# Kernel optimization log

Measured on AMD Instinct MI355X. Metric: run time of the kernel, lower is better.

Reference implementation:

```python
import jax, jax.numpy as jnp
import numpy as np

EMB, NH, NG, T_MAX = 2048, 16, 4, 2048
HD = EMB // NH          # 128
HPG = NH // NG          # 4
B, T = 2, 2048


def _rope_tables(t):
    inv_freq = 1.0 / (10000.0 ** (jnp.arange(0, HD, 2, dtype=jnp.float32) / HD))
    freqs = jnp.outer(jnp.arange(t, dtype=jnp.float32), inv_freq)  # [t, HD//2]
    return jnp.cos(freqs), jnp.sin(freqs)


def _apply_rope(x, cos, sin):
    # x: [..., t, HD], interleaved pairs (0::2 real, 1::2 imag)
    x1 = x[..., 0::2]
    x2 = x[..., 1::2]
    r1 = x1 * cos - x2 * sin
    r2 = x1 * sin + x2 * cos
    return jnp.stack([r1, r2], axis=-1).reshape(x.shape)


def setup_inputs() -> dict:
    key = jax.random.key(0)
    ks = jax.random.split(key, 5)
    s = 0.02
    return {
        "x": jax.random.normal(ks[0], (B, T, EMB), dtype=jnp.float32),
        "Wq": jax.random.normal(ks[1], (EMB, EMB), dtype=jnp.float32) * s,
        "Wk": jax.random.normal(ks[2], (NG * HD, EMB), dtype=jnp.float32) * s,
        "Wv": jax.random.normal(ks[3], (NG * HD, EMB), dtype=jnp.float32) * s,
        "Wo": jax.random.normal(ks[4], (EMB, EMB), dtype=jnp.float32) * s,
    }


def reference(x, Wq, Wk, Wv, Wo):
    b, t, _ = x.shape
    cos, sin = _rope_tables(t)  # [t, HD//2] each; broadcast over batch/heads

    # projections (torch Linear: x @ W.T)
    q = (x @ Wq.T).reshape(b, t, NH, HD).transpose(0, 2, 1, 3)  # [b, NH, t, HD]
    k = (x @ Wk.T).reshape(b, t, NG, HD).transpose(0, 2, 1, 3)  # [b, NG, t, HD]
    v = (x @ Wv.T).reshape(b, t, NG, HD).transpose(0, 2, 1, 3)  # [b, NG, t, HD]

    q = _apply_rope(q, cos, sin)
    k = _apply_rope(k, cos, sin)

    # grouped attention without materializing expanded K/V
    qg = q.reshape(b, NG, HPG, t, HD)                       # [b, g, h, t, d]
    scale = 1.0 / jnp.sqrt(jnp.asarray(HD, dtype=x.dtype))
    scores = jnp.einsum('bghtd,bgsd->bghts', qg, k) * scale  # [b, g, h, t, s]

    causal = jnp.tril(jnp.ones((t, t), dtype=bool))
    scores = jnp.where(causal, scores, jnp.finfo(scores.dtype).min)
    attn = jax.nn.softmax(scores, axis=-1)

    out = jnp.einsum('bghts,bgsd->bghtd', attn, v)           # [b, g, h, t, d]
    out = out.reshape(b, NH, t, HD).transpose(0, 2, 1, 3).reshape(b, t, EMB)
    return out @ Wo.T
```

## Files before the change

### kernel.cpp

```cpp
#include <hip/hip_runtime.h>
#include <stdint.h>
#include <math.h>

#define EMB 2048
#define NHq 16
#define NGk 4
#define HD 128
#define Bb 2
#define Tt 2048
#define MROWS (Bb*Tt)
#define QKVN 3072
#define NQT 32

typedef __bf16 bf16x8 __attribute__((ext_vector_type(8)));
typedef float f32x4 __attribute__((ext_vector_type(4)));
typedef unsigned int u32x4 __attribute__((ext_vector_type(4)));
typedef unsigned short u16;
typedef unsigned int u32;

__device__ __forceinline__ u16 f2bf(float f) {
    unsigned int u = __float_as_uint(f);
    u += 0x7fff + ((u >> 16) & 1);
    return (u16)(u >> 16);
}
__device__ __forceinline__ float bf2f(u16 u) {
    return __uint_as_float(((u32)u) << 16);
}
__device__ __forceinline__ u32 cvt_pk_bf16(float lo, float hi) {
    u32 r;
    asm("v_cvt_pk_bf16_f32 %0, %1, %2" : "=v"(r) : "v"(lo), "v"(hi));
    return r;
}

#define GLOAD_LDS16(g, l) \
    __builtin_amdgcn_global_load_lds((const __attribute__((address_space(1))) void*)(g), \
                                     (__attribute__((address_space(3))) void*)(l), 16, 0, 0)

__global__ void cast_bf16_kernel(const float* __restrict__ src, u16* __restrict__ dst, int n4) {
    int i = blockIdx.x * blockDim.x + threadIdx.x;
    if (i < n4) {
        float4 v = reinterpret_cast<const float4*>(src)[i];
        ushort4 o;
        o.x = f2bf(v.x); o.y = f2bf(v.y); o.z = f2bf(v.z); o.w = f2bf(v.w);
        reinterpret_cast<ushort4*>(dst)[i] = o;
    }
}

__global__ void wcast_kernel(const float* __restrict__ Wq, const float* __restrict__ Wk,
                             const float* __restrict__ Wv, const float* __restrict__ Wo,
                             u16* __restrict__ dst) {
    int i = blockIdx.x * blockDim.x + threadIdx.x;
    const float* src; int local;
    if (i < 1048576)      { src = Wq; local = i; }
    else if (i < 1310720) { src = Wk; local = i - 1048576; }
    else if (i < 1572864) { src = Wv; local = i - 1310720; }
    else                  { src = Wo; local = i - 1572864; }
    float4 v = reinterpret_cast<const float4*>(src)[local];
    ushort4 o;
    o.x = f2bf(v.x); o.y = f2bf(v.y); o.z = f2bf(v.z); o.w = f2bf(v.w);
    reinterpret_cast<ushort4*>(dst)[i] = o;
}

__global__ void rope_tables_kernel(float* __restrict__ ctab, float* __restrict__ stab) {
    int t = blockIdx.x, i = threadIdx.x;
    float inv = powf(10000.f, -2.f * (float)i / (float)HD);
    float ang = (float)t * inv;
    ctab[t * 64 + i] = cosf(ang);
    stab[t * 64 + i] = sinf(ang);
}

__global__ void rope_qk_kernel(const u16* __restrict__ lin, const float* __restrict__ ctab,
                               const float* __restrict__ stab, u16* __restrict__ Qb,
                               u16* __restrict__ Kb, float qscale) {
    int i = threadIdx.x;
    int tt = blockIdx.x * 4 + threadIdx.y;
    int hh = blockIdx.y, b = blockIdx.z;
    int coloff; u16* out; float scale;
    if (hh < NHq) { coloff = hh * HD; scale = qscale;
                    out = Qb + (((size_t)(b * NHq + hh)) * Tt + tt) * HD; }
    else { int g = hh - NHq; coloff = EMB + g * HD; scale = 1.f;
           out = Kb + (((size_t)(b * NGk + g)) * Tt + tt) * HD; }
    u32 pair = *reinterpret_cast<const u32*>(&lin[((size_t)(b * Tt + tt)) * QKVN + coloff + 2 * i]);
    float x1 = bf2f((u16)(pair & 0xffff)), x2 = bf2f((u16)(pair >> 16));
    float c = ctab[tt * 64 + i], s = stab[tt * 64 + i];
    ushort2 o;
    o.x = f2bf((x1 * c - x2 * s) * scale);
    o.y = f2bf((x1 * s + x2 * c) * scale);
    *reinterpret_cast<ushort2*>(&out[2 * i]) = o;
}

__global__ void vtrans_kernel(const u16* __restrict__ lin, u16* __restrict__ vt) {
    int tx = threadIdx.x, dy = threadIdx.y;
    int tt = blockIdx.x * 64 + tx;
    int g = blockIdx.y, b = blockIdx.z;
    int ttp = (tt & ~31) | (((tt >> 2) & 3) * 8 + ((tt >> 4) & 1) * 4 + (tt & 3));
    const u16* src = &lin[((size_t)(b * Tt + tt)) * QKVN + EMB + NGk * HD + g * HD];
    u16* dst = &vt[(((size_t)(b * NGk + g)) * HD) * Tt + ttp];
    #pragma unroll
    for (int k = 0; k < 16; ++k) {
        int d = dy + k * 8;
        dst[(size_t)d * Tt] = src[d];
    }
}

template<int OUTBF>
__global__ __launch_bounds__(256) void gemm_bt(const u16* __restrict__ A, const u16* __restrict__ W,
                                               void* __restrict__ Cout, int M, int N, int K) {
    __shared__ u16 Atile[128 * 32];
    __shared__ u16 Btile[128 * 32];
    const int brow = blockIdx.x * 128;
    const int bcol = blockIdx.y * 128;
    const int t = threadIdx.x;
    const int w = t >> 6, l = t & 63;
    const int lr = l & 15, lq = l >> 4;
    const int wr = (w >> 1) * 64, wc = (w & 1) * 64;
    f32x4 acc[4][4] = {};
    const int nkt = K >> 5;
    for (int kt = 0; kt < nkt; ++kt) {
        const int k0 = kt * 32;
        #pragma unroll
        for (int i = 0; i < 2; ++i) {
            int f = i * 256 + t;
            int row = f >> 2, cb = (f & 3) * 8;
            GLOAD_LDS16(A + (size_t)(brow + row) * K + k0 + cb, &Atile[(i * 256 + w * 64) * 8]);
            GLOAD_LDS16(W + (size_t)(bcol + row) * K + k0 + cb, &Btile[(i * 256 + w * 64) * 8]);
        }
        __syncthreads();
        bf16x8 a[4], b[4];
        #pragma unroll
        for (int m = 0; m < 4; ++m)
            a[m] = *reinterpret_cast<const bf16x8*>(&Atile[(wr + m * 16 + lr) * 32 + lq * 8]);
        #pragma unroll
        for (int n = 0; n < 4; ++n)
            b[n] = *reinterpret_cast<const bf16x8*>(&Btile[(wc + n * 16 + lr) * 32 + lq * 8]);
        #pragma unroll
        for (int m = 0; m < 4; ++m)
            #pragma unroll
            for (int n = 0; n < 4; ++n)
                acc[m][n] = __builtin_amdgcn_mfma_f32_16x16x32_bf16(a[m], b[n], acc[m][n], 0, 0, 0);
        __syncthreads();
    }
    #pragma unroll
    for (int m = 0; m < 4; ++m)
        #pragma unroll
        for (int n = 0; n < 4; ++n)
            #pragma unroll
            for (int r = 0; r < 4; ++r) {
                size_t idx = (size_t)(brow + wr + m * 16 + lq * 4 + r) * N + bcol + wc + n * 16 + lr;
                if (OUTBF) ((u16*)Cout)[idx] = f2bf(acc[m][n][r]);
                else       ((float*)Cout)[idx] = acc[m][n][r];
            }
}

__global__ __launch_bounds__(256) void flash_attn(const u16* __restrict__ Q, const u16* __restrict__ K,
                                                  const u16* __restrict__ Vt, u16* __restrict__ Out) {
    __shared__ __align__(16) char smem[65536];
    const int h = blockIdx.y;
    const int b = blockIdx.z;
    const int qt = (b == 0) ? blockIdx.x : (15 - blockIdx.x);
    const int g = h >> 2;
    const int t = threadIdx.x;
    const int w = t >> 6, l = t & 63;
    const int lr = l & 15, lq = l >> 4;
    const int qbase = qt * 128 + w * 32;

    const size_t qhead = ((size_t)(b * NHq + h)) * Tt;
    bf16x8 qf0[4], qf1[4];
    #pragma unroll
    for (int d = 0; d < 4; ++d) {
        qf0[d] = *reinterpret_cast<const bf16x8*>(&Q[(qhead + qbase + lr) * HD + d * 32 + lq * 8]);
        qf1[d] = *reinterpret_cast<const bf16x8*>(&Q[(qhead + qbase + 16 + lr) * HD + d * 32 + lq * 8]);
    }
    bf16x8 ones;
    #pragma unroll
    for (int j = 0; j < 8; ++j) ones[j] = (__bf16)1.0f;

    f32x4 o0[8] = {}, o1[8] = {};
    f32x4 ls0 = {}, ls1 = {};

    const int q0 = qbase + lr;
    const int q1 = qbase + 16 + lr;
    const int lastvis = (qbase + 31) >> 6;
    const size_t kbase  = ((size_t)(b * NGk + g)) * Tt * HD;
    const size_t vtbase = ((size_t)(b * NGk + g)) * HD * Tt;
    const int nkt = 2 * (qt + 1);

    int kofs[4], vofs[4];
    #pragma unroll
    for (int j = 0; j < 4; ++j) {
        int krow = j * 16 + (t >> 4);
        kofs[j] = krow * HD + (((t & 15) ^ (krow & 7)) * 8);
        int vrow = j * 32 + (t >> 3);
        vofs[j] = vrow * (int)Tt + (((t & 7) ^ (vrow & 7)) * 8);
    }

    #pragma unroll
    for (int j = 0; j < 4; ++j) {
        GLOAD_LDS16(K + kbase + kofs[j], smem + (j * 256 + t) * 16);
        GLOAD_LDS16(Vt + vtbase + vofs[j], smem + 32768 + (j * 256 + t) * 16);
    }

    for (int kt = 0; kt < nkt; ++kt) {
        __syncthreads();
        if (kt + 1 < nkt) {
            const size_t kp1 = (size_t)(kt + 1) * 64;
            char* kd = smem + ((kt + 1) & 1) * 16384;
            char* vd = smem + 32768 + ((kt + 1) & 1) * 16384;
            #pragma unroll
            for (int j = 0; j < 4; ++j) {
                GLOAD_LDS16(K + kbase + kp1 * HD + kofs[j], kd + (j * 256 + t) * 16);
                GLOAD_LDS16(Vt + vtbase + kp1 + vofs[j], vd + (j * 256 + t) * 16);
            }
        }
        if (kt > lastvis) continue;
        const char* Kb = smem + (kt & 1) * 16384;
        const char* Vb = smem + 32768 + (kt & 1) * 16384;

        f32x4 s0[4] = {}, s1[4] = {};
        __builtin_amdgcn_s_setprio(1);
        #pragma unroll
        for (int ct = 0; ct < 4; ++ct) {
            #pragma unroll
            for (int d = 0; d < 4; ++d) {
                int row = ct * 16 + lr;
                int bo = row * 256 + ((d * 64 + lq * 16) ^ ((row & 7) << 4));
                bf16x8 kf = *reinterpret_cast<const bf16x8*>(Kb + bo);
                s0[ct] = __builtin_amdgcn_mfma_f32_16x16x32_bf16(kf, qf0[d], s0[ct], 0, 0, 0);
                s1[ct] = __builtin_amdgcn_mfma_f32_16x16x32_bf16(kf, qf1[d], s1[ct], 0, 0, 0);
            }
        }
        __builtin_amdgcn_s_setprio(0);

        const bool diag = (kt == lastvis);
        const int kvb = kt * 64 + lq * 4;
        bf16x8 pf0[2], pf1[2];
        {
            float e[4][4];
            #pragma unroll
            for (int ct = 0; ct < 4; ++ct)
                #pragma unroll
                for (int r = 0; r < 4; ++r)
                    e[ct][r] = exp2f(s0[ct][r]);
            if (diag) {
                #pragma unroll
                for (int ct = 0; ct < 4; ++ct)
                    #pragma unroll
                    for (int r = 0; r < 4; ++r)
                        if (kvb + ct * 16 + r > q0) e[ct][r] = 0.f;
            }
            #pragma unroll
            for (int ks = 0; ks < 2; ++ks) {
                u32x4 pk;
                pk[0] = cvt_pk_bf16(e[ks * 2][0], e[ks * 2][1]);
                pk[1] = cvt_pk_bf16(e[ks * 2][2], e[ks * 2][3]);
                pk[2] = cvt_pk_bf16(e[ks * 2 + 1][0], e[ks * 2 + 1][1]);
                pk[3] = cvt_pk_bf16(e[ks * 2 + 1][2], e[ks * 2 + 1][3]);
                pf0[ks] = __builtin_bit_cast(bf16x8, pk);
            }
        }
        {
            float e[4][4];
            #pragma unroll
            for (int ct = 0; ct < 4; ++ct)
                #pragma unroll
                for (int r = 0; r < 4; ++r)
                    e[ct][r] = exp2f(s1[ct][r]);
            if (diag) {
                #pragma unroll
                for (int ct = 0; ct < 4; ++ct)
                    #pragma unroll
                    for (int r = 0; r < 4; ++r)
                        if (kvb + ct * 16 + r > q1) e[ct][r] = 0.f;
            }
            #pragma unroll
            for (int ks = 0; ks < 2; ++ks) {
                u32x4 pk;
                pk[0] = cvt_pk_bf16(e[ks * 2][0], e[ks * 2][1]);
                pk[1] = cvt_pk_bf16(e[ks * 2][2], e[ks * 2][3]);
                pk[2] = cvt_pk_bf16(e[ks * 2 + 1][0], e[ks * 2 + 1][1]);
                pk[3] = cvt_pk_bf16(e[ks * 2 + 1][2], e[ks * 2 + 1][3]);
                pf1[ks] = __builtin_bit_cast(bf16x8, pk);
            }
        }

        __builtin_amdgcn_s_setprio(1);
        #pragma unroll
        for (int n = 0; n < 8; ++n) {
            int vrow = n * 16 + lr;
            #pragma unroll
            for (int ks = 0; ks < 2; ++ks) {
                int bv = vrow * 128 + ((ks * 64 + lq * 16) ^ ((vrow & 7) << 4));
                bf16x8 vf = *reinterpret_cast<const bf16x8*>(Vb + bv);
                o0[n] = __builtin_amdgcn_mfma_f32_16x16x32_bf16(vf, pf0[ks], o0[n], 0, 0, 0);
                o1[n] = __builtin_amdgcn_mfma_f32_16x16x32_bf16(vf, pf1[ks], o1[n], 0, 0, 0);
            }
        }
        ls0 = __builtin_amdgcn_mfma_f32_16x16x32_bf16(ones, pf0[0], ls0, 0, 0, 0);
        ls0 = __builtin_amdgcn_mfma_f32_16x16x32_bf16(ones, pf0[1], ls0, 0, 0, 0);
        ls1 = __builtin_amdgcn_mfma_f32_16x16x32_bf16(ones, pf1[0], ls1, 0, 0, 0);
        ls1 = __builtin_amdgcn_mfma_f32_16x16x32_bf16(ones, pf1[1], ls1, 0, 0, 0);
        __builtin_amdgcn_s_setprio(0);
    }

    {
        const float inv0 = 1.f / ls0[0];
        const float inv1 = 1.f / ls1[0];
        u16* out0 = Out + ((size_t)(b * Tt) + q0) * EMB + h * HD;
        u16* out1 = Out + ((size_t)(b * Tt) + q1) * EMB + h * HD;
        #pragma unroll
        for (int n = 0; n < 8; ++n) {
            uint2 p0, p1;
            p0.x = cvt_pk_bf16(o0[n][0] * inv0, o0[n][1] * inv0);
            p0.y = cvt_pk_bf16(o0[n][2] * inv0, o0[n][3] * inv0);
            p1.x = cvt_pk_bf16(o1[n][0] * inv1, o1[n][1] * inv1);
            p1.y = cvt_pk_bf16(o1[n][2] * inv1, o1[n][3] * inv1);
            *reinterpret_cast<uint2*>(&out0[n * 16 + lq * 4]) = p0;
            *reinterpret_cast<uint2*>(&out1[n * 16 + lq * 4]) = p1;
        }
    }
}

extern "C" void kernel_launch(void* const* d_in, const int* in_sizes, int n_in,
                              void* d_out, int out_size, void* d_ws, size_t ws_size,
                              hipStream_t stream) {
    (void)in_sizes; (void)n_in; (void)out_size; (void)ws_size;
    const float* x  = (const float*)d_in[0];
    const float* Wq = (const float*)d_in[1];
    const float* Wk = (const float*)d_in[2];
    const float* Wv = (const float*)d_in[3];
    const float* Wo = (const float*)d_in[4];
    float* out = (float*)d_out;

    char* ws = (char*)d_ws;
    size_t off = 0;
    auto alloc = [&](size_t bytes) { char* p = ws + off; off += (bytes + 255) & ~(size_t)255; return p; };

    u16* w_bf    = (u16*)alloc((size_t)(QKVN * EMB + EMB * EMB) * 2);
    u16* x_bf    = (u16*)alloc((size_t)MROWS * EMB * 2);
    u16* qkv_lin = (u16*)alloc((size_t)MROWS * QKVN * 4);
    u16* Qb      = (u16*)alloc((size_t)Bb * NHq * Tt * HD * 2);
    u16* Kb      = (u16*)alloc((size_t)Bb * NGk * Tt * HD * 2);
    u16* Vtb     = (u16*)alloc((size_t)Bb * NGk * HD * Tt * 2);
    float* ctab  = (float*)alloc((size_t)Tt * 64 * 4);
    float* stab  = (float*)alloc((size_t)Tt * 64 * 4);
    u16* attnout = qkv_lin;

    u16* wo_bf = w_bf + (size_t)QKVN * EMB;

    cast_bf16_kernel<<<(MROWS * EMB / 4 + 255) / 256, 256, 0, stream>>>(x, x_bf, MROWS * EMB / 4);
    wcast_kernel<<<(QKVN * EMB + EMB * EMB) / 4 / 256, 256, 0, stream>>>(Wq, Wk, Wv, Wo, w_bf);
    rope_tables_kernel<<<Tt, 64, 0, stream>>>(ctab, stab);

    gemm_bt<1><<<dim3(MROWS / 128, QKVN / 128), 256, 0, stream>>>(x_bf, w_bf, qkv_lin, MROWS, QKVN, EMB);

    const float qscale = 1.44269504088896f / sqrtf((float)HD);
    rope_qk_kernel<<<dim3(Tt / 4, NHq + NGk, Bb), dim3(64, 4), 0, stream>>>(qkv_lin, ctab, stab, Qb, Kb, qscale);
    vtrans_kernel<<<dim3(Tt / 64, NGk, Bb), dim3(64, 8), 0, stream>>>(qkv_lin, Vtb);

    flash_attn<<<dim3(16, NHq, Bb), 256, 0, stream>>>(Qb, Kb, Vtb, attnout);

    gemm_bt<0><<<dim3(MROWS / 128, EMB / 128), 256, 0, stream>>>(attnout, wo_bf, out, MROWS, EMB, EMB);
}
```

Before: 233.2 us.

## Replace 128x128 GEMM with double-buffered 256x256 tile GEMM using swizzled LDS

Replaces the simple 128x128, K=32 single-buffered GEMM with a 512-thread kernel on 256x256 output tiles and K=64 steps. The next K tile is loaded into a second LDS buffer while MFMAs run on the current one, with vmcnt waits and priority raising around the compute phases. The LDS layout gets an XOR swizzle to avoid bank conflicts, and the workgroup order is remapped for L2 locality. The larger tiles cut global traffic and barrier overhead per FLOP. The cost is 128KB of LDS and a large register footprint, which limit occupancy, and the grid shrinks to 192 and 128 workgroups, so the machine may be underfilled.

```diff
diff --git a/kernel.cpp b/kernel.cpp
--- a/kernel.cpp
+++ b/kernel.cpp
@@ -35,6 +35,9 @@
 #define GLOAD_LDS16(g, l) \
     __builtin_amdgcn_global_load_lds((const __attribute__((address_space(1))) void*)(g), \
                                      (__attribute__((address_space(3))) void*)(l), 16, 0, 0)
+#define FENCE asm volatile("" ::: "memory")
+#define BARRIER { FENCE; __builtin_amdgcn_s_barrier(); FENCE; }
+#define VMCNT(n) asm volatile("s_waitcnt vmcnt(" #n ")")
 
 __global__ void cast_bf16_kernel(const float* __restrict__ src, u16* __restrict__ dst, int n4) {
     int i = blockIdx.x * blockDim.x + threadIdx.x;
@@ -104,52 +107,107 @@
 }
 
 template<int OUTBF>
-__global__ __launch_bounds__(256) void gemm_bt(const u16* __restrict__ A, const u16* __restrict__ W,
+__global__ __launch_bounds__(512) void gemm256(const u16* __restrict__ A, const u16* __restrict__ W,
                                                void* __restrict__ Cout, int M, int N, int K) {
-    __shared__ u16 Atile[128 * 32];
-    __shared__ u16 Btile[128 * 32];
-    const int brow = blockIdx.x * 128;
-    const int bcol = blockIdx.y * 128;
+    __shared__ __align__(16) char smem[131072];
+    const int nbm = M >> 8;
+    const int nwg = gridDim.x;
+    const int cpx = nwg >> 3;
+    const int swz = ((int)blockIdx.x & 7) * cpx + ((int)blockIdx.x >> 3);
+    const int brow = (swz % nbm) << 8;
+    const int bcol = (swz / nbm) << 8;
     const int t = threadIdx.x;
-    const int w = t >> 6, l = t & 63;
-    const int lr = l & 15, lq = l >> 4;
-    const int wr = (w >> 1) * 64, wc = (w & 1) * 64;
-    f32x4 acc[4][4] = {};
-    const int nkt = K >> 5;
+    const int l = t & 63, lr = l & 15, lq = l >> 4;
+    const int w = t >> 6, wm = w >> 2, wn = w & 3;
+
+    int srow[4], scol[4];
+    #pragma unroll
+    for (int j = 0; j < 4; ++j) {
+        int p = (j * 512 + t) * 16;
+        int e = p ^ (((p >> 9) & 1) << 5);
+        srow[j] = e >> 7;
+        scol[j] = (e & 127) >> 1;
+    }
+
+#define STG_A(d, kt, h) { \
+    GLOAD_LDS16(A + (size_t)(brow + srow[(h)*2]) * K + (size_t)(kt) * 64 + scol[(h)*2], \
+                smem + (d) * 65536 + ((h)*2 * 512 + t) * 16); \
+    GLOAD_LDS16(A + (size_t)(brow + srow[(h)*2+1]) * K + (size_t)(kt) * 64 + scol[(h)*2+1], \
+                smem + (d) * 65536 + (((h)*2+1) * 512 + t) * 16); }
+#define STG_B(d, kt, h) { \
+    GLOAD_LDS16(W + (size_t)(bcol + srow[(h)*2]) * K + (size_t)(kt) * 64 + scol[(h)*2], \
+                smem + (d) * 65536 + 32768 + ((h)*2 * 512 + t) * 16); \
+    GLOAD_LDS16(W + (size_t)(bcol + srow[(h)*2+1]) * K + (size_t)(kt) * 64 + scol[(h)*2+1], \
+                smem + (d) * 65536 + 32768 + (((h)*2+1) * 512 + t) * 16); }
+
+    f32x4 acc[8][4] = {};
+    const int nkt = K >> 6;
+
+    STG_A(0, 0, 0); STG_B(0, 0, 0); STG_B(0, 0, 1); STG_A(0, 0, 1);
+    VMCNT(4); BARRIER;
+
     for (int kt = 0; kt < nkt; ++kt) {
-        const int k0 = kt * 32;
+        const int cur = kt & 1, nxt = cur ^ 1;
+        const bool more = (kt + 1 < nkt);
         #pragma unroll
-        for (int i = 0; i < 2; ++i) {
-            int f = i * 256 + t;
-            int row = f >> 2, cb = (f & 3) * 8;
-            GLOAD_LDS16(A + (size_t)(brow + row) * K + k0 + cb, &Atile[(i * 256 + w * 64) * 8]);
-            GLOAD_LDS16(W + (size_t)(bcol + row) * K + k0 + cb, &Btile[(i * 256 + w * 64) * 8]);
-        }
-        __syncthreads();
-        bf16x8 a[4], b[4];
-        #pragma unroll
-        for (int m = 0; m < 4; ++m)
-            a[m] = *reinterpret_cast<const bf16x8*>(&Atile[(wr + m * 16 + lr) * 32 + lq * 8]);
+        for (int ph = 0; ph < 4; ++ph) {
+            const int mh = ph >> 1, nh = ph & 1;
+            bf16x8 af[4][2], bfr[2][2];
+            #pragma unroll
+            for (int m = 0; m < 4; ++m)
+                #pragma unroll
+                for (int kk = 0; kk < 2; ++kk) {
+                    int lin = (wm * 128 + (mh * 4 + m) * 16 + lr) * 128 + kk * 64 + lq * 16;
+                    af[m][kk] = *reinterpret_cast<const bf16x8*>(
+                        smem + cur * 65536 + (lin ^ (((lin >> 9) & 1) << 5)));
+                }
+            #pragma unroll
+            for (int n = 0; n < 2; ++n)
+                #pragma unroll
+                for (int kk = 0; kk < 2; ++kk) {
+                    int lin = (wn * 64 + (nh * 2 + n) * 16 + lr) * 128 + kk * 64 + lq * 16;
+                    bfr[n][kk] = *reinterpret_cast<const bf16x8*>(
+                        smem + cur * 65536 + 32768 + (lin ^ (((lin >> 9) & 1) << 5)));
+                }
+            if (more) {
+                if (ph == 0) STG_A(nxt, kt + 1, 0)
+                else if (ph == 1) STG_B(nxt, kt + 1, 0)
+                else if (ph == 2) STG_B(nxt, kt + 1, 1)
+                else STG_A(nxt, kt + 1, 1)
+            }
+            if (more) {
+                if (ph != 2) VMCNT(4);
+            } else {
+                if (ph == 0) VMCNT(2);
+                else if (ph == 1) VMCNT(0);
+            }
+            BARRIER;
+            __builtin_amdgcn_s_setprio(1);
+            #pragma unroll
+            for (int m = 0; m < 4; ++m)
+                #pragma unroll
+                for (int n = 0; n < 2; ++n)
+                    #pragma unroll
+                    for (int kk = 0; kk < 2; ++kk)
+                        acc[mh * 4 + m][nh * 2 + n] = __builtin_amdgcn_mfma_f32_16x16x32_bf16(
+                            af[m][kk], bfr[n][kk], acc[mh * 4 + m][nh * 2 + n], 0, 0, 0);
+            __builtin_amdgcn_s_setprio(0);
+            BARRIER;
+        }
+    }
+
+    #pragma unroll
+    for (int m = 0; m < 8; ++m)
         #pragma unroll
         for (int n = 0; n < 4; ++n)
-            b[n] = *reinterpret_cast<const bf16x8*>(&Btile[(wc + n * 16 + lr) * 32 + lq * 8]);
-        #pragma unroll
-        for (int m = 0; m < 4; ++m)
-            #pragma unroll
-            for (int n = 0; n < 4; ++n)
-                acc[m][n] = __builtin_amdgcn_mfma_f32_16x16x32_bf16(a[m], b[n], acc[m][n], 0, 0, 0);
-        __syncthreads();
-    }
-    #pragma unroll
-    for (int m = 0; m < 4; ++m)
-        #pragma unroll
-        for (int n = 0; n < 4; ++n)
             #pragma unroll
             for (int r = 0; r < 4; ++r) {
-                size_t idx = (size_t)(brow + wr + m * 16 + lq * 4 + r) * N + bcol + wc + n * 16 + lr;
+                size_t idx = (size_t)(brow + wm * 128 + m * 16 + lq * 4 + r) * N + bcol + wn * 64 + n * 16 + lr;
                 if (OUTBF) ((u16*)Cout)[idx] = f2bf(acc[m][n][r]);
                 else       ((float*)Cout)[idx] = acc[m][n][r];
             }
+#undef STG_A
+#undef STG_B
 }
 
 __global__ __launch_bounds__(256) void flash_attn(const u16* __restrict__ Q, const u16* __restrict__ K,
@@ -351,7 +409,7 @@
     wcast_kernel<<<(QKVN * EMB + EMB * EMB) / 4 / 256, 256, 0, stream>>>(Wq, Wk, Wv, Wo, w_bf);
     rope_tables_kernel<<<Tt, 64, 0, stream>>>(ctab, stab);
 
-    gemm_bt<1><<<dim3(MROWS / 128, QKVN / 128), 256, 0, stream>>>(x_bf, w_bf, qkv_lin, MROWS, QKVN, EMB);
+    gemm256<1><<<dim3((MROWS / 256) * (QKVN / 256)), 512, 0, stream>>>(x_bf, w_bf, qkv_lin, MROWS, QKVN, EMB);
 
     const float qscale = 1.44269504088896f / sqrtf((float)HD);
     rope_qk_kernel<<<dim3(Tt / 4, NHq + NGk, Bb), dim3(64, 4), 0, stream>>>(qkv_lin, ctab, stab, Qb, Kb, qscale);
@@ -359,5 +417,5 @@
 
     flash_attn<<<dim3(16, NHq, Bb), 256, 0, stream>>>(Qb, Kb, Vtb, attnout);
 
-    gemm_bt<0><<<dim3(MROWS / 128, EMB / 128), 256, 0, stream>>>(attnout, wo_bf, out, MROWS, EMB, EMB);
-}
+    gemm256<0><<<dim3((MROWS / 256) * (EMB / 256)), 512, 0, stream>>>(attnout, wo_bf, out, MROWS, EMB, EMB);
+}
```

After: 275.2 us. 1.18x slower.

## Add 256x256-tile pipelined GEMM with XOR-swizzled LDS for QKV projection

Applied to the files above, without the earlier changes.

Adds a new bf16 GEMM kernel with 256x256 output tiles, 512 threads and a double-buffered 128KB LDS that is filled via direct global-to-LDS loads. Loads are split into interleaved quarter stages with explicit vmcnt waits and barriers, and MFMA bursts run at raised priority. It also adds an XOR swizzle against LDS bank conflicts and a grouped block-index remap for L2 locality. Only the QKV projection uses it; the larger tiles raise data reuse per block, but the grid shrinks to 192 blocks and the heavy LDS use limits occupancy to one block per CU.

```diff
diff --git a/kernel.cpp b/kernel.cpp
--- a/kernel.cpp
+++ b/kernel.cpp
@@ -35,6 +35,9 @@
 #define GLOAD_LDS16(g, l) \
     __builtin_amdgcn_global_load_lds((const __attribute__((address_space(1))) void*)(g), \
                                      (__attribute__((address_space(3))) void*)(l), 16, 0, 0)
+#define FENCE asm volatile("" ::: "memory")
+#define BARRIER { FENCE; __builtin_amdgcn_s_barrier(); FENCE; }
+#define VMCNT(n) asm volatile("s_waitcnt vmcnt(" #n ")")
 
 __global__ void cast_bf16_kernel(const float* __restrict__ src, u16* __restrict__ dst, int n4) {
     int i = blockIdx.x * blockDim.x + threadIdx.x;
@@ -152,6 +155,115 @@
             }
 }
 
+template<int OUTBF>
+__global__ __launch_bounds__(512) void gemm256(const u16* __restrict__ A, const u16* __restrict__ W,
+                                               void* __restrict__ Cout, int M, int N, int K) {
+    __shared__ __align__(16) char smem[131072];
+    const int nbm = M >> 8;
+    const int nwg = gridDim.x;
+    const int cpx = nwg >> 3;
+    const int swz = ((int)blockIdx.x & 7) * cpx + ((int)blockIdx.x >> 3);
+    const int brow = (swz % nbm) << 8;
+    const int bcol = (swz / nbm) << 8;
+    const int t = threadIdx.x;
+    const int l = t & 63, lr = l & 15, lq = l >> 4;
+    const int w = t >> 6, wm = w >> 2, wn = w & 3;
+
+    int lrj[2], slj[2], sej[2];
+    #pragma unroll
+    for (int j = 0; j < 2; ++j) {
+        int c = j * 512 + t;
+        lrj[j] = c >> 3; slj[j] = c & 7; sej[j] = (c & 7) ^ ((c >> 3) & 7);
+    }
+
+#define STGA(d, kt1, h) { \
+    _Pragma("unroll") \
+    for (int j = 0; j < 2; ++j) { \
+        int row = (lrj[j] & 63) + (h) * 64 + (lrj[j] >> 6) * 128; \
+        GLOAD_LDS16(A + (size_t)(brow + row) * K + (size_t)(kt1) * 64 + sej[j] * 8, \
+                    smem + (d) * 65536 + row * 128 + slj[j] * 16); } }
+#define STGB(d, kt1, h) { \
+    _Pragma("unroll") \
+    for (int j = 0; j < 2; ++j) { \
+        int row = (lrj[j] & 31) + (h) * 32 + (lrj[j] >> 5) * 64; \
+        GLOAD_LDS16(W + (size_t)(bcol + row) * K + (size_t)(kt1) * 64 + sej[j] * 8, \
+                    smem + (d) * 65536 + 32768 + row * 128 + slj[j] * 16); } }
+#define RDA(cur, mh) { \
+    _Pragma("unroll") \
+    for (int m = 0; m < 4; ++m) \
+        _Pragma("unroll") \
+        for (int kk = 0; kk < 2; ++kk) { \
+            int row = wm * 128 + (mh) * 64 + m * 16 + lr; \
+            int slr = (kk * 4 + lq) ^ (lr & 7); \
+            af[m][kk] = *reinterpret_cast<const bf16x8*>(smem + (cur) * 65536 + row * 128 + slr * 16); } }
+#define RDB(cur, nh, bq) { \
+    _Pragma("unroll") \
+    for (int n = 0; n < 2; ++n) \
+        _Pragma("unroll") \
+        for (int kk = 0; kk < 2; ++kk) { \
+            int row = wn * 64 + (nh) * 32 + n * 16 + lr; \
+            int slr = (kk * 4 + lq) ^ (lr & 7); \
+            bq[n][kk] = *reinterpret_cast<const bf16x8*>(smem + (cur) * 65536 + 32768 + row * 128 + slr * 16); } }
+#define MM(bq, mo, no) { \
+    __builtin_amdgcn_s_setprio(1); \
+    _Pragma("unroll") \
+    for (int m = 0; m < 4; ++m) \
+        _Pragma("unroll") \
+        for (int n = 0; n < 2; ++n) \
+            _Pragma("unroll") \
+            for (int kk = 0; kk < 2; ++kk) \
+                acc[(mo) + m][(no) + n] = __builtin_amdgcn_mfma_f32_16x16x32_bf16( \
+                    af[m][kk], bq[n][kk], acc[(mo) + m][(no) + n], 0, 0, 0); \
+    __builtin_amdgcn_s_setprio(0); }
+
+    f32x4 acc[8][4] = {};
+    bf16x8 af[4][2], b0[2][2], b1[2][2];
+    const int nkt = K >> 6;
+
+    STGA(0, 0, 0); STGB(0, 0, 0); STGB(0, 0, 1); STGA(0, 0, 1);
+    VMCNT(4); BARRIER;
+
+    for (int kt = 0; kt < nkt; ++kt) {
+        const int cur = kt & 1, nxt = cur ^ 1;
+        const bool more = (kt + 1 < nkt);
+        RDA(cur, 0); RDB(cur, 0, b0);
+        if (more) { STGA(nxt, kt + 1, 0); VMCNT(4); } else { VMCNT(2); }
+        BARRIER;
+        MM(b0, 0, 0);
+        BARRIER;
+        RDB(cur, 1, b1);
+        if (more) { STGB(nxt, kt + 1, 0); VMCNT(4); } else { VMCNT(0); }
+        BARRIER;
+        MM(b1, 0, 2);
+        BARRIER;
+        RDA(cur, 1);
+        if (more) STGB(nxt, kt + 1, 1);
+        BARRIER;
+        MM(b0, 4, 0);
+        BARRIER;
+        if (more) { STGA(nxt, kt + 1, 1); VMCNT(4); }
+        BARRIER;
+        MM(b1, 4, 2);
+        BARRIER;
+    }
+
+    #pragma unroll
+    for (int m = 0; m < 8; ++m)
+        #pragma unroll
+        for (int n = 0; n < 4; ++n)
+            #pragma unroll
+            for (int r = 0; r < 4; ++r) {
+                size_t idx = (size_t)(brow + wm * 128 + m * 16 + lq * 4 + r) * N + bcol + wn * 64 + n * 16 + lr;
+                if (OUTBF) ((u16*)Cout)[idx] = f2bf(acc[m][n][r]);
+                else       ((float*)Cout)[idx] = acc[m][n][r];
+            }
+#undef STGA
+#undef STGB
+#undef RDA
+#undef RDB
+#undef MM
+}
+
 __global__ __launch_bounds__(256) void flash_attn(const u16* __restrict__ Q, const u16* __restrict__ K,
                                                   const u16* __restrict__ Vt, u16* __restrict__ Out) {
     __shared__ __align__(16) char smem[65536];
@@ -351,7 +463,7 @@
     wcast_kernel<<<(QKVN * EMB + EMB * EMB) / 4 / 256, 256, 0, stream>>>(Wq, Wk, Wv, Wo, w_bf);
     rope_tables_kernel<<<Tt, 64, 0, stream>>>(ctab, stab);
 
-    gemm_bt<1><<<dim3(MROWS / 128, QKVN / 128), 256, 0, stream>>>(x_bf, w_bf, qkv_lin, MROWS, QKVN, EMB);
+    gemm256<1><<<dim3((MROWS / 256) * (QKVN / 256)), 512, 0, stream>>>(x_bf, w_bf, qkv_lin, MROWS, QKVN, EMB);
 
     const float qscale = 1.44269504088896f / sqrtf((float)HD);
     rope_qk_kernel<<<dim3(Tt / 4, NHq + NGk, Bb), dim3(64, 4), 0, stream>>>(qkv_lin, ctab, stab, Qb, Kb, qscale);
```

Result: faster. 221.6 us, median of 3 (-5.0%).
